# Kernel optimization log

Measured on AMD Instinct MI355X. Metric: run time of the kernel, lower is better.

Reference implementation:

```python
import jax, jax.numpy as jnp
import numpy as np

B, S, D = 4, 4096, 64

def setup_inputs() -> dict:
    key = jax.random.key(0)
    kq, kk, kv = jax.random.split(key, 3)
    q = jax.random.normal(kq, (B, S, D), dtype=jnp.float32)
    k = jax.random.normal(kk, (B, S, D), dtype=jnp.float32)
    v = jax.random.normal(kv, (B, S, D), dtype=jnp.float32)
    return {"q": q, "k": k, "v": v}

def reference(q, k, v):
    d_k = k.shape[-1]
    # scores: [B, S, S]
    scores = jnp.einsum('bqd,bkd->bqk', q, k) / jnp.sqrt(jnp.asarray(d_k, q.dtype))
    s = scores.shape[-1]
    # causal mask: disallow j > i (strict upper triangle)
    causal = jnp.tril(jnp.ones((scores.shape[-2], s), dtype=bool))
    scores = jnp.where(causal, scores, jnp.asarray(-jnp.inf, scores.dtype))
    norm_scores = jax.nn.softmax(scores, axis=-1)
    return jnp.einsum('bqk,bkd->bqd', norm_scores, v)
```

## Files before the change

### kernel.cpp

```cpp
#include <hip/hip_runtime.h>

#define B_ 4
#define S_ 4096
#define D_ 64

typedef __attribute__((ext_vector_type(8))) short short8;
typedef __attribute__((ext_vector_type(4))) float f32x4;
typedef __attribute__((ext_vector_type(16))) float f32x16;
typedef __attribute__((ext_vector_type(4))) int int4v;
typedef __attribute__((ext_vector_type(2))) unsigned uint2v;
typedef unsigned short u16;

__device__ __forceinline__ unsigned pack_bf2(float a, float b) {
  unsigned ua = __float_as_uint(a) + 0x8000u;
  unsigned ub = __float_as_uint(b) + 0x8000u;
  return __builtin_amdgcn_perm(ub, ua, 0x07060302);
}

__device__ __forceinline__ float fexp2(float x) {
#if __has_builtin(__builtin_amdgcn_exp2f)
  return __builtin_amdgcn_exp2f(x);
#else
  return exp2f(x);
#endif
}

__device__ __forceinline__ uint2v permswap(unsigned a, unsigned b) {
#if __has_builtin(__builtin_amdgcn_permlane32_swap)
  return __builtin_amdgcn_permlane32_swap(a, b, false, false);
#else
  int h = (threadIdx.x >> 5) & 1;
  unsigned ta = __shfl_xor(a, 32);
  unsigned tb = __shfl_xor(b, 32);
  uint2v r;
  r[0] = h ? tb : a;
  r[1] = h ? b : ta;
  return r;
#endif
}

__global__ __launch_bounds__(256) void cvt_all_k(const float* __restrict__ q,
                                                 const float* __restrict__ k,
                                                 const float* __restrict__ v,
                                                 u16* __restrict__ wsQ,
                                                 u16* __restrict__ wsK,
                                                 u16* __restrict__ wsV) {
  int blk = blockIdx.x;
  if (blk < 1024) {
    const float* src = (blk < 512) ? q : k;
    u16* dst = (blk < 512) ? wsQ : wsK;
    float scale = (blk < 512) ? 0.18033688011112042f : 1.0f;
    int t = ((blk & 511) << 8) + threadIdx.x;
    const f32x4* s4 = (const f32x4*)src;
    f32x4 a = s4[2 * t], b = s4[2 * t + 1];
    int4v r;
    r[0] = (int)pack_bf2(a[0] * scale, a[1] * scale);
    r[1] = (int)pack_bf2(a[2] * scale, a[3] * scale);
    r[2] = (int)pack_bf2(b[0] * scale, b[1] * scale);
    r[3] = (int)pack_bf2(b[2] * scale, b[3] * scale);
    *(int4v*)(dst + 8 * (long)t) = r;
  } else {
    int t = ((blk - 1024) << 8) + threadIdx.x;
    int lane = t & 63;
    int J  = (t >> 6) & 3;
    int dt = (t >> 8) & 1;
    int ck = (t >> 9) & 63;
    int b  = t >> 15;
    int row = ck * 64 + J * 16 + (lane >> 5) * 8;
    int col = dt * 32 + (lane & 31);
    const float* src = v + ((long)(b * S_ + row)) * D_ + col;
    float e[8];
#pragma unroll
    for (int i = 0; i < 8; i++) e[i] = src[(long)i * D_];
    int4v r;
    r[0] = (int)pack_bf2(e[0], e[1]);
    r[1] = (int)pack_bf2(e[2], e[3]);
    r[2] = (int)pack_bf2(e[4], e[5]);
    r[3] = (int)pack_bf2(e[6], e[7]);
    *(int4v*)(wsV + 8 * (long)t) = r;
  }
}

#define MFMA32(a, bb, cc) __builtin_amdgcn_mfma_f32_32x32x16_bf16((a), (bb), (cc), 0, 0, 0)

__global__ __launch_bounds__(512, 2) void attn_k(const u16* __restrict__ wsQ,
                                                 const u16* __restrict__ wsK,
                                                 const u16* __restrict__ wsV,
                                                 float* __restrict__ out) {
  int bid = blockIdx.x;
  int b   = bid & 3;
  int g32 = 127 - (bid >> 2);
  int tid = threadIdx.x;
  int w = tid >> 6, lane = tid & 63, c2 = lane & 31, h = lane >> 5;
  int cmax = g32 >> 1;
  int q0 = g32 * 32;
  int dq = 32 * (g32 & 1) + c2;

  __shared__ float sMem[8][2176];
  __shared__ float sML[8][32];

  float* W = &sMem[w][0];

  short8 qf[4];
#pragma unroll
  for (int kk = 0; kk < 4; kk++)
    qf[kk] = *(const short8*)(wsQ + ((long)(b * S_ + q0 + c2)) * D_ + kk * 16 + h * 8);

  f32x16 o0, o1;
#pragma unroll
  for (int r = 0; r < 16; r++) { o0[r] = 0.f; o1[r] = 0.f; }
  float lp = 0.f;

  const u16* kbase = wsK + ((long)(b * S_ + c2)) * D_ + h * 8;
  const u16* vbase = wsV + ((long)(b * 64)) * 4096 + (long)lane * 8;

  auto loadKV = [&](short8 (&kf)[2][4], short8 (&vf)[2][4], int ck) {
    const u16* kp = kbase + (long)ck * 64 * D_;
#pragma unroll
    for (int jt = 0; jt < 2; jt++)
#pragma unroll
      for (int kk = 0; kk < 4; kk++)
        kf[jt][kk] = *(const short8*)(kp + jt * 32 * D_ + kk * 16);
    const u16* vp = vbase + (long)ck * 4096;
#pragma unroll
    for (int dt = 0; dt < 2; dt++)
#pragma unroll
      for (int J = 0; J < 4; J++)
        vf[dt][J] = *(const short8*)(vp + (dt * 4 + J) * 512);
  };

  auto compute = [&](short8 (&kf)[2][4], short8 (&vf)[2][4], int ck) {
    f32x16 s[2];
#pragma unroll
    for (int r = 0; r < 16; r++) { s[0][r] = 0.f; s[1][r] = 0.f; }
#pragma unroll
    for (int kk = 0; kk < 4; kk++) {
      s[0] = MFMA32(kf[0][kk], qf[kk], s[0]);
      s[1] = MFMA32(kf[1][kk], qf[kk], s[1]);
    }

    if (ck == cmax) {
#pragma unroll
      for (int r = 0; r < 16; r++) {
        int row = (r & 3) + 8 * (r >> 2) + 4 * h;
        if (row      > dq) s[0][r] = -1e30f;
        if (row + 32 > dq) s[1][r] = -1e30f;
      }
    }

    float su0 = 0.f, su1 = 0.f, su2 = 0.f, su3 = 0.f;
#pragma unroll
    for (int r = 0; r < 4; r++) {
      s[0][r]      = fexp2(s[0][r]);      su0 += s[0][r];
      s[0][r + 4]  = fexp2(s[0][r + 4]);  su1 += s[0][r + 4];
      s[0][r + 8]  = fexp2(s[0][r + 8]);  su2 += s[0][r + 8];
      s[0][r + 12] = fexp2(s[0][r + 12]); su3 += s[0][r + 12];
    }
#pragma unroll
    for (int r = 0; r < 4; r++) {
      s[1][r]      = fexp2(s[1][r]);      su0 += s[1][r];
      s[1][r + 4]  = fexp2(s[1][r + 4]);  su1 += s[1][r + 4];
      s[1][r + 8]  = fexp2(s[1][r + 8]);  su2 += s[1][r + 8];
      s[1][r + 12] = fexp2(s[1][r + 12]); su3 += s[1][r + 12];
    }
    lp += (su0 + su1) + (su2 + su3);

    short8 p[4];
#pragma unroll
    for (int jt = 0; jt < 2; jt++) {
      unsigned Dw[8];
#pragma unroll
      for (int g = 0; g < 4; g++) {
        Dw[2 * g]     = pack_bf2(s[jt][4 * g],     s[jt][4 * g + 1]);
        Dw[2 * g + 1] = pack_bf2(s[jt][4 * g + 2], s[jt][4 * g + 3]);
      }
#pragma unroll
      for (int e = 0; e < 2; e++) {
        uint2v r0 = permswap(Dw[4 * e],     Dw[4 * e + 2]);
        uint2v r1 = permswap(Dw[4 * e + 1], Dw[4 * e + 3]);
        int4v pw;
        pw[0] = (int)r0[0]; pw[1] = (int)r1[0];
        pw[2] = (int)r0[1]; pw[3] = (int)r1[1];
        p[2 * jt + e] = __builtin_bit_cast(short8, pw);
      }
    }

#pragma unroll
    for (int J = 0; J < 4; J++) {
      o0 = MFMA32(vf[0][J], p[J], o0);
      o1 = MFMA32(vf[1][J], p[J], o1);
    }
  };

  short8 kfA[2][4], vfA[2][4], kfB[2][4], vfB[2][4];
  int ck0 = w;
  if (ck0 <= cmax) loadKV(kfA, vfA, ck0);
  for (int ck = ck0; ck <= cmax; ck += 16) {
    int ckB = ck + 8;
    if (ckB <= cmax) loadKV(kfB, vfB, ckB);
    compute(kfA, vfA, ck);
    int ckA2 = ck + 16;
    if (ckA2 <= cmax) loadKV(kfA, vfA, ckA2);
    if (ckB <= cmax) compute(kfB, vfB, ckB);
  }

  lp += __shfl_xor(lp, 32);
  if (h == 0) sML[w][c2] = lp;
#pragma unroll
  for (int dt = 0; dt < 2; dt++)
#pragma unroll
    for (int grp = 0; grp < 4; grp++) {
      f32x4 t4;
      const f32x16& ov = dt ? o1 : o0;
      t4[0] = ov[4 * grp]; t4[1] = ov[4 * grp + 1];
      t4[2] = ov[4 * grp + 2]; t4[3] = ov[4 * grp + 3];
      *(f32x4*)&W[c2 * 68 + 32 * dt + 8 * grp + 4 * h] = t4;
    }
  __syncthreads();

  int q = tid >> 4, d4 = tid & 15;
  float L = 0.f;
  f32x4 acc = {0.f, 0.f, 0.f, 0.f};
#pragma unroll
  for (int w2 = 0; w2 < 8; w2++) {
    L += sML[w2][q];
    f32x4 pv = *(f32x4*)&sMem[w2][q * 68 + d4 * 4];
#pragma unroll
    for (int i = 0; i < 4; i++) acc[i] += pv[i];
  }
  float inv = 1.f / L;
  f32x4 r;
#pragma unroll
  for (int i = 0; i < 4; i++) r[i] = acc[i] * inv;
  *(f32x4*)(out + ((long)(b * S_ + q0 + q)) * D_ + d4 * 4) = r;
}

extern "C" void kernel_launch(void* const* d_in, const int* in_sizes, int n_in,
                              void* d_out, int out_size, void* d_ws, size_t ws_size,
                              hipStream_t stream) {
  const float* q = (const float*)d_in[0];
  const float* k = (const float*)d_in[1];
  const float* v = (const float*)d_in[2];
  float* out = (float*)d_out;

  u16* wsQ = (u16*)d_ws;
  u16* wsK = wsQ + (long)B_ * S_ * D_;
  u16* wsV = wsK + (long)B_ * S_ * D_;

  cvt_all_k<<<1536, 256, 0, stream>>>(q, k, v, wsQ, wsK, wsV);
  attn_k<<<512, 512, 0, stream>>>(wsQ, wsK, wsV, out);
}
```

Measured before the change: 92.58 us.

## Process 64 query rows per block to reuse K/V fragments across two tiles

Each block now handles two 32-row query tiles, so every K/V fragment loaded from global memory feeds both tiles. The grid halves to 256 blocks. The explicit A/B register double-buffering of K/V loads is removed in favour of a simple per-chunk loop. This halves K/V global traffic per query row, but it doubles accumulator registers, leaves fewer blocks than the 256 CUs can fully occupy, and loses the manual load/compute overlap.

```diff
diff --git a/kernel.cpp b/kernel.cpp
--- a/kernel.cpp
+++ b/kernel.cpp
@@ -89,150 +89,152 @@
                                                  float* __restrict__ out) {
   int bid = blockIdx.x;
   int b   = bid & 3;
-  int g32 = 127 - (bid >> 2);
+  int g   = 63 - (bid >> 2);
   int tid = threadIdx.x;
   int w = tid >> 6, lane = tid & 63, c2 = lane & 31, h = lane >> 5;
-  int cmax = g32 >> 1;
-  int q0 = g32 * 32;
-  int dq = 32 * (g32 & 1) + c2;
+  int cmax = g;
+  int q0 = g * 64;
 
   __shared__ float sMem[8][2176];
-  __shared__ float sML[8][32];
+  __shared__ float sML[8][2][32];
 
   float* W = &sMem[w][0];
 
-  short8 qf[4];
-#pragma unroll
-  for (int kk = 0; kk < 4; kk++)
-    qf[kk] = *(const short8*)(wsQ + ((long)(b * S_ + q0 + c2)) * D_ + kk * 16 + h * 8);
-
-  f32x16 o0, o1;
-#pragma unroll
-  for (int r = 0; r < 16; r++) { o0[r] = 0.f; o1[r] = 0.f; }
-  float lp = 0.f;
+  short8 qf[2][4];
+#pragma unroll
+  for (int t = 0; t < 2; t++)
+#pragma unroll
+    for (int kk = 0; kk < 4; kk++)
+      qf[t][kk] = *(const short8*)(wsQ + ((long)(b * S_ + q0 + 32 * t + c2)) * D_ +
+                                   kk * 16 + h * 8);
+
+  f32x16 o[2][2];
+#pragma unroll
+  for (int t = 0; t < 2; t++)
+#pragma unroll
+    for (int dt = 0; dt < 2; dt++)
+#pragma unroll
+      for (int r = 0; r < 16; r++) o[t][dt][r] = 0.f;
+  float lp[2] = {0.f, 0.f};
 
   const u16* kbase = wsK + ((long)(b * S_ + c2)) * D_ + h * 8;
   const u16* vbase = wsV + ((long)(b * 64)) * 4096 + (long)lane * 8;
 
-  auto loadKV = [&](short8 (&kf)[2][4], short8 (&vf)[2][4], int ck) {
+  for (int ck = w; ck <= cmax; ck += 8) {
     const u16* kp = kbase + (long)ck * 64 * D_;
+    short8 kf[2][4];
 #pragma unroll
     for (int jt = 0; jt < 2; jt++)
 #pragma unroll
       for (int kk = 0; kk < 4; kk++)
         kf[jt][kk] = *(const short8*)(kp + jt * 32 * D_ + kk * 16);
     const u16* vp = vbase + (long)ck * 4096;
+    short8 vf[2][4];
 #pragma unroll
     for (int dt = 0; dt < 2; dt++)
 #pragma unroll
       for (int J = 0; J < 4; J++)
         vf[dt][J] = *(const short8*)(vp + (dt * 4 + J) * 512);
-  };
-
-  auto compute = [&](short8 (&kf)[2][4], short8 (&vf)[2][4], int ck) {
-    f32x16 s[2];
-#pragma unroll
-    for (int r = 0; r < 16; r++) { s[0][r] = 0.f; s[1][r] = 0.f; }
-#pragma unroll
-    for (int kk = 0; kk < 4; kk++) {
-      s[0] = MFMA32(kf[0][kk], qf[kk], s[0]);
-      s[1] = MFMA32(kf[1][kk], qf[kk], s[1]);
+
+#pragma unroll
+    for (int t = 0; t < 2; t++) {
+      f32x16 s[2];
+#pragma unroll
+      for (int r = 0; r < 16; r++) { s[0][r] = 0.f; s[1][r] = 0.f; }
+#pragma unroll
+      for (int kk = 0; kk < 4; kk++) {
+        s[0] = MFMA32(kf[0][kk], qf[t][kk], s[0]);
+        s[1] = MFMA32(kf[1][kk], qf[t][kk], s[1]);
+      }
+
+      if (ck == cmax) {
+        int dq = 32 * t + c2;
+#pragma unroll
+        for (int r = 0; r < 16; r++) {
+          int row = (r & 3) + 8 * (r >> 2) + 4 * h;
+          if (row      > dq) s[0][r] = -1e30f;
+          if (row + 32 > dq) s[1][r] = -1e30f;
+        }
+      }
+
+      float su0 = 0.f, su1 = 0.f, su2 = 0.f, su3 = 0.f;
+#pragma unroll
+      for (int r = 0; r < 4; r++) {
+        s[0][r]      = fexp2(s[0][r]);      su0 += s[0][r];
+        s[0][r + 4]  = fexp2(s[0][r + 4]);  su1 += s[0][r + 4];
+        s[0][r + 8]  = fexp2(s[0][r + 8]);  su2 += s[0][r + 8];
+        s[0][r + 12] = fexp2(s[0][r + 12]); su3 += s[0][r + 12];
+        s[1][r]      = fexp2(s[1][r]);      su0 += s[1][r];
+        s[1][r + 4]  = fexp2(s[1][r + 4]);  su1 += s[1][r + 4];
+        s[1][r + 8]  = fexp2(s[1][r + 8]);  su2 += s[1][r + 8];
+        s[1][r + 12] = fexp2(s[1][r + 12]); su3 += s[1][r + 12];
+      }
+      lp[t] += (su0 + su1) + (su2 + su3);
+
+      short8 p[4];
+#pragma unroll
+      for (int jt = 0; jt < 2; jt++) {
+        unsigned Dw[8];
+#pragma unroll
+        for (int gg = 0; gg < 4; gg++) {
+          Dw[2 * gg]     = pack_bf2(s[jt][4 * gg],     s[jt][4 * gg + 1]);
+          Dw[2 * gg + 1] = pack_bf2(s[jt][4 * gg + 2], s[jt][4 * gg + 3]);
+        }
+#pragma unroll
+        for (int e = 0; e < 2; e++) {
+          uint2v r0 = permswap(Dw[4 * e],     Dw[4 * e + 2]);
+          uint2v r1 = permswap(Dw[4 * e + 1], Dw[4 * e + 3]);
+          int4v pw;
+          pw[0] = (int)r0[0]; pw[1] = (int)r1[0];
+          pw[2] = (int)r0[1]; pw[3] = (int)r1[1];
+          p[2 * jt + e] = __builtin_bit_cast(short8, pw);
+        }
+      }
+
+#pragma unroll
+      for (int J = 0; J < 4; J++) {
+        o[t][0] = MFMA32(vf[0][J], p[J], o[t][0]);
+        o[t][1] = MFMA32(vf[1][J], p[J], o[t][1]);
+      }
     }
-
-    if (ck == cmax) {
-#pragma unroll
-      for (int r = 0; r < 16; r++) {
-        int row = (r & 3) + 8 * (r >> 2) + 4 * h;
-        if (row      > dq) s[0][r] = -1e30f;
-        if (row + 32 > dq) s[1][r] = -1e30f;
-      }
+  }
+
+#pragma unroll
+  for (int t = 0; t < 2; t++) {
+    float lt = lp[t];
+    lt += __shfl_xor(lt, 32);
+    if (h == 0) sML[w][t][c2] = lt;
+  }
+
+  for (int t = 0; t < 2; t++) {
+    __syncthreads();
+#pragma unroll
+    for (int dt = 0; dt < 2; dt++)
+#pragma unroll
+      for (int grp = 0; grp < 4; grp++) {
+        f32x4 t4;
+        t4[0] = o[t][dt][4 * grp];     t4[1] = o[t][dt][4 * grp + 1];
+        t4[2] = o[t][dt][4 * grp + 2]; t4[3] = o[t][dt][4 * grp + 3];
+        *(f32x4*)&W[c2 * 68 + 32 * dt + 8 * grp + 4 * h] = t4;
+      }
+    __syncthreads();
+
+    int q = tid >> 4, d4 = tid & 15;
+    float L = 0.f;
+    f32x4 acc = {0.f, 0.f, 0.f, 0.f};
+#pragma unroll
+    for (int w2 = 0; w2 < 8; w2++) {
+      L += sML[w2][t][q];
+      f32x4 pv = *(f32x4*)&sMem[w2][q * 68 + d4 * 4];
+#pragma unroll
+      for (int i = 0; i < 4; i++) acc[i] += pv[i];
     }
-
-    float su0 = 0.f, su1 = 0.f, su2 = 0.f, su3 = 0.f;
-#pragma unroll
-    for (int r = 0; r < 4; r++) {
-      s[0][r]      = fexp2(s[0][r]);      su0 += s[0][r];
-      s[0][r + 4]  = fexp2(s[0][r + 4]);  su1 += s[0][r + 4];
-      s[0][r + 8]  = fexp2(s[0][r + 8]);  su2 += s[0][r + 8];
-      s[0][r + 12] = fexp2(s[0][r + 12]); su3 += s[0][r + 12];
-    }
-#pragma unroll
-    for (int r = 0; r < 4; r++) {
-      s[1][r]      = fexp2(s[1][r]);      su0 += s[1][r];
-      s[1][r + 4]  = fexp2(s[1][r + 4]);  su1 += s[1][r + 4];
-      s[1][r + 8]  = fexp2(s[1][r + 8]);  su2 += s[1][r + 8];
-      s[1][r + 12] = fexp2(s[1][r + 12]); su3 += s[1][r + 12];
-    }
-    lp += (su0 + su1) + (su2 + su3);
-
-    short8 p[4];
-#pragma unroll
-    for (int jt = 0; jt < 2; jt++) {
-      unsigned Dw[8];
-#pragma unroll
-      for (int g = 0; g < 4; g++) {
-        Dw[2 * g]     = pack_bf2(s[jt][4 * g],     s[jt][4 * g + 1]);
-        Dw[2 * g + 1] = pack_bf2(s[jt][4 * g + 2], s[jt][4 * g + 3]);
-      }
-#pragma unroll
-      for (int e = 0; e < 2; e++) {
-        uint2v r0 = permswap(Dw[4 * e],     Dw[4 * e + 2]);
-        uint2v r1 = permswap(Dw[4 * e + 1], Dw[4 * e + 3]);
-        int4v pw;
-        pw[0] = (int)r0[0]; pw[1] = (int)r1[0];
-        pw[2] = (int)r0[1]; pw[3] = (int)r1[1];
-        p[2 * jt + e] = __builtin_bit_cast(short8, pw);
-      }
-    }
-
-#pragma unroll
-    for (int J = 0; J < 4; J++) {
-      o0 = MFMA32(vf[0][J], p[J], o0);
-      o1 = MFMA32(vf[1][J], p[J], o1);
-    }
-  };
-
-  short8 kfA[2][4], vfA[2][4], kfB[2][4], vfB[2][4];
-  int ck0 = w;
-  if (ck0 <= cmax) loadKV(kfA, vfA, ck0);
-  for (int ck = ck0; ck <= cmax; ck += 16) {
-    int ckB = ck + 8;
-    if (ckB <= cmax) loadKV(kfB, vfB, ckB);
-    compute(kfA, vfA, ck);
-    int ckA2 = ck + 16;
-    if (ckA2 <= cmax) loadKV(kfA, vfA, ckA2);
-    if (ckB <= cmax) compute(kfB, vfB, ckB);
-  }
-
-  lp += __shfl_xor(lp, 32);
-  if (h == 0) sML[w][c2] = lp;
-#pragma unroll
-  for (int dt = 0; dt < 2; dt++)
-#pragma unroll
-    for (int grp = 0; grp < 4; grp++) {
-      f32x4 t4;
-      const f32x16& ov = dt ? o1 : o0;
-      t4[0] = ov[4 * grp]; t4[1] = ov[4 * grp + 1];
-      t4[2] = ov[4 * grp + 2]; t4[3] = ov[4 * grp + 3];
-      *(f32x4*)&W[c2 * 68 + 32 * dt + 8 * grp + 4 * h] = t4;
-    }
-  __syncthreads();
-
-  int q = tid >> 4, d4 = tid & 15;
-  float L = 0.f;
-  f32x4 acc = {0.f, 0.f, 0.f, 0.f};
-#pragma unroll
-  for (int w2 = 0; w2 < 8; w2++) {
-    L += sML[w2][q];
-    f32x4 pv = *(f32x4*)&sMem[w2][q * 68 + d4 * 4];
-#pragma unroll
-    for (int i = 0; i < 4; i++) acc[i] += pv[i];
-  }
-  float inv = 1.f / L;
-  f32x4 r;
-#pragma unroll
-  for (int i = 0; i < 4; i++) r[i] = acc[i] * inv;
-  *(f32x4*)(out + ((long)(b * S_ + q0 + q)) * D_ + d4 * 4) = r;
+    float inv = 1.f / L;
+    f32x4 r;
+#pragma unroll
+    for (int i = 0; i < 4; i++) r[i] = acc[i] * inv;
+    *(f32x4*)(out + ((long)(b * S_ + q0 + 32 * t + q)) * D_ + d4 * 4) = r;
+  }
 }
 
 extern "C" void kernel_launch(void* const* d_in, const int* in_sizes, int n_in,
@@ -248,5 +250,5 @@
   u16* wsV = wsK + (long)B_ * S_ * D_;
 
   cvt_all_k<<<1536, 256, 0, stream>>>(q, k, v, wsQ, wsK, wsV);
-  attn_k<<<512, 512, 0, stream>>>(wsQ, wsK, wsV, out);
-}
+  attn_k<<<256, 512, 0, stream>>>(wsQ, wsK, wsV, out);
+}
```

After: 92.17 us. No clear change (-0.4%).
